# Performance work log

Measured on AMD Instinct MI355X. Metric: run time of the kernel, lower is better.

The kernel has to match this reference:

```python
import jax, jax.numpy as jnp
import numpy as np

B, S, DIM, H = 2, 2048, 1024, 16
DK = DIM // H  # 64
NEG = -10000000000.0


def setup_inputs() -> dict:
    key = jax.random.key(0)
    k1, k2, k3, k4, k5, k6 = jax.random.split(key, 6)
    dec_xs = jax.random.normal(k1, (B, S, DIM), dtype=jnp.float32)
    enc_xs = jax.random.normal(k2, (B, S, DIM), dtype=jnp.float32)
    mask = jax.random.randint(k3, (B, S, S), 0, 2, dtype=jnp.int32)
    # torch Linear weights: out = x @ W.T, bias=False
    sc = 1.0 / np.sqrt(DIM)
    Wq = jax.random.normal(k4, (DIM, DIM), dtype=jnp.float32) * sc
    Wkv = jax.random.normal(k5, (2 * DIM, DIM), dtype=jnp.float32) * sc
    Wo = jax.random.normal(k6, (DIM, DIM), dtype=jnp.float32) * sc
    return {"dec_xs": dec_xs, "enc_xs": enc_xs, "Wq": Wq, "Wkv": Wkv, "Wo": Wo, "mask": mask}


def reference(dec_xs, enc_xs, Wq, Wkv, Wo, mask):
    b, s, dim = enc_xs.shape
    qs = dec_xs @ Wq.T                      # [b,s,dim]  (dropout inactive in eval)
    kv = enc_xs @ Wkv.T                     # [b,s,2*dim]
    ks, vs = jnp.split(kv, 2, axis=-1)
    # head layout: view(b, s, dk, h) -- heads LAST, as in the original
    qs = qs.reshape(b, s, DK, H)
    ks = ks.reshape(b, s, DK, H)
    vs = vs.reshape(b, s, DK, H)
    scores = jnp.einsum('bqdh,bkdh->bqkh', qs, ks) / np.sqrt(DK)
    scores = jnp.where(mask[..., None] == 0, NEG, scores)
    weights = jax.nn.softmax(scores, axis=-2)  # softmax over key axis
    out = jnp.einsum('bqkh,bkdh->bqdh', weights, vs).reshape(b, s, dim)
    return out @ Wo.T
```

## Files before the change

kernel.cpp:

```cpp
#include <hip/hip_runtime.h>
#include <hip/hip_bf16.h>

#define BB 2
#define SS 2048
#define DIMM 1024
#define HH 16
#define DKK 64
#define QSCALE 0.18033688011112042592f

using bf16 = __hip_bfloat16;
typedef __attribute__((ext_vector_type(8))) short v8s;
typedef __attribute__((ext_vector_type(4))) short v4s;
typedef __attribute__((ext_vector_type(4))) float f32x4;

__device__ __forceinline__ void cvt4(const float* __restrict__ s,
                                     bf16* __restrict__ d, int idx) {
  const float4 f = ((const float4*)s)[idx];
  bf16 t[4] = {__float2bfloat16(f.x), __float2bfloat16(f.y),
               __float2bfloat16(f.z), __float2bfloat16(f.w)};
  *(v4s*)(d + (size_t)idx * 4) = *(const v4s*)t;
}

__global__ __launch_bounds__(256) void convert_pack_kernel(
    const float* __restrict__ dec, const float* __restrict__ enc,
    const float* __restrict__ Wq, const float* __restrict__ Wkv,
    const float* __restrict__ Wo, const int* __restrict__ mask,
    bf16* __restrict__ decb, bf16* __restrict__ encb, bf16* __restrict__ Wqb,
    bf16* __restrict__ Wkvb, bf16* __restrict__ Wob,
    unsigned long long* __restrict__ mp) {
  const int gid = blockIdx.x * 256 + threadIdx.x;
  const int NT = 256 * 1024;
#pragma unroll
  for (int i = 0; i < 4; ++i) cvt4(dec, decb, gid + i * NT);
#pragma unroll
  for (int i = 0; i < 4; ++i) cvt4(enc, encb, gid + i * NT);
  cvt4(Wq, Wqb, gid);
#pragma unroll
  for (int i = 0; i < 2; ++i) cvt4(Wkv, Wkvb, gid + i * NT);
  {
    const int n = gid >> 8;
    const int c4 = (gid & 255) * 4;
    const int h = c4 >> 6, d0 = c4 & 63;
    const float* src = Wo + (size_t)n * DIMM + h;
    bf16 t[4];
#pragma unroll
    for (int i2 = 0; i2 < 4; ++i2)
      t[i2] = __float2bfloat16(src[(d0 + i2) * 16]);
    *(v4s*)(Wob + (size_t)n * DIMM + c4) = *(const v4s*)t;
  }
  const int lane = threadIdx.x & 63;
  const int wave_id = gid >> 6;
  for (int i = 0; i < 32; ++i) {
    const size_t w = (size_t)wave_id * 32 + i;
    const unsigned long long bm = __ballot(mask[w * 64 + lane] != 0);
    if (lane == 0) mp[w] = bm;
  }
}

__global__ __launch_bounds__(256) void proj_gemm_kernel(
    const bf16* __restrict__ decb, const bf16* __restrict__ encb,
    const bf16* __restrict__ Wqb, const bf16* __restrict__ Wkvb,
    bf16* __restrict__ Qr, bf16* __restrict__ Kr, bf16* __restrict__ Vt) {
  __shared__ __align__(16) bf16 As[128][72];
  __shared__ __align__(16) bf16 Bs[128][72];
  const int t = threadIdx.x;
  const int wave = t >> 6, lane = t & 63;
  const int quad = lane >> 4, l15 = lane & 15;
  const int wm = (wave >> 1) * 64, wn = (wave & 1) * 64;
  const int bx = blockIdx.x;
  const int kind = bx >> 3;
  const int g = bx & 7;
  const int m0 = blockIdx.y * 128;

  const int sr = t >> 2;
  const int sc = (t & 3) * 16;
  const int voff = (kind == 2) ? DIMM : 0;
  const int wr0 = sr * 16 + g * 2 + voff;
  const int wr1 = sr * 16 + g * 2 + 1 + voff;

  const bf16* arow0;
  const bf16* arow1;
  const bf16* brow0;
  const bf16* brow1;
  if (kind == 0) {
    arow0 = decb + (size_t)(m0 + sr) * DIMM;
    arow1 = decb + (size_t)(m0 + sr + 64) * DIMM;
    brow0 = Wqb + (size_t)wr0 * DIMM;
    brow1 = Wqb + (size_t)wr1 * DIMM;
  } else if (kind == 1) {
    arow0 = encb + (size_t)(m0 + sr) * DIMM;
    arow1 = encb + (size_t)(m0 + sr + 64) * DIMM;
    brow0 = Wkvb + (size_t)wr0 * DIMM;
    brow1 = Wkvb + (size_t)wr1 * DIMM;
  } else {
    arow0 = Wkvb + (size_t)wr0 * DIMM;
    arow1 = Wkvb + (size_t)wr1 * DIMM;
    brow0 = encb + (size_t)(m0 + sr) * DIMM;
    brow1 = encb + (size_t)(m0 + sr + 64) * DIMM;
  }

  v8s apf[4], bpf[4];
  auto loadAB = [&](int kc) {
    apf[0] = ((const v8s*)(arow0 + kc + sc))[0];
    apf[1] = ((const v8s*)(arow0 + kc + sc))[1];
    apf[2] = ((const v8s*)(arow1 + kc + sc))[0];
    apf[3] = ((const v8s*)(arow1 + kc + sc))[1];
    bpf[0] = ((const v8s*)(brow0 + kc + sc))[0];
    bpf[1] = ((const v8s*)(brow0 + kc + sc))[1];
    bpf[2] = ((const v8s*)(brow1 + kc + sc))[0];
    bpf[3] = ((const v8s*)(brow1 + kc + sc))[1];
  };

  f32x4 acc[4][4] = {};
  loadAB(0);

  for (int kc = 0; kc < DIMM; kc += 64) {
    __syncthreads();
    *(v8s*)&As[sr][sc] = apf[0];
    *(v8s*)&As[sr][sc + 8] = apf[1];
    *(v8s*)&As[sr + 64][sc] = apf[2];
    *(v8s*)&As[sr + 64][sc + 8] = apf[3];
    *(v8s*)&Bs[sr][sc] = bpf[0];
    *(v8s*)&Bs[sr][sc + 8] = bpf[1];
    *(v8s*)&Bs[sr + 64][sc] = bpf[2];
    *(v8s*)&Bs[sr + 64][sc + 8] = bpf[3];
    if (kc + 64 < DIMM) loadAB(kc + 64);
    __syncthreads();
#pragma unroll
    for (int ks = 0; ks < 2; ++ks) {
      v8s af[4], bfr[4];
#pragma unroll
      for (int i = 0; i < 4; ++i)
        af[i] = *(const v8s*)&As[wm + i * 16 + l15][ks * 32 + quad * 8];
#pragma unroll
      for (int j = 0; j < 4; ++j)
        bfr[j] = *(const v8s*)&Bs[wn + j * 16 + l15][ks * 32 + quad * 8];
#pragma unroll
      for (int i = 0; i < 4; ++i)
#pragma unroll
        for (int j = 0; j < 4; ++j)
          acc[i][j] = __builtin_amdgcn_mfma_f32_16x16x32_bf16(
              af[i], bfr[j], acc[i][j], 0, 0, 0);
    }
  }

#pragma unroll
  for (int i = 0; i < 4; ++i) {
#pragma unroll
    for (int r = 0; r < 4; ++r) {
      const int mm = wm + i * 16 + quad * 4 + r;
#pragma unroll
      for (int j = 0; j < 4; ++j) {
        const int nn = wn + j * 16 + l15;
        const float v = acc[i][j][r];
        if (kind == 0) {
          Qr[(size_t)(m0 + mm) * DIMM + g * 128 + nn] =
              __float2bfloat16(v * QSCALE);
        } else if (kind == 1) {
          Kr[(size_t)(m0 + mm) * DIMM + g * 128 + nn] = __float2bfloat16(v);
        } else {
          const int h = g * 2 + (mm >> 6), d = mm & 63;
          const int sn = m0 + nn;
          const int b = sn >> 11, s = sn & (SS - 1);
          Vt[(((size_t)b * HH + h) * DKK + d) * SS + s] = __float2bfloat16(v);
        }
      }
    }
  }
}

__global__ __launch_bounds__(256) void out_gemm_kernel(
    const bf16* __restrict__ A, const bf16* __restrict__ W,
    float* __restrict__ out) {
  __shared__ __align__(16) bf16 As[128][72];
  __shared__ __align__(16) bf16 Bs[64][72];
  const int t = threadIdx.x;
  const int wave = t >> 6, lane = t & 63;
  const int quad = lane >> 4, l15 = lane & 15;
  const int wm = (wave >> 1) * 64, wn = (wave & 1) * 32;
  const int n0 = blockIdx.x * 64;
  const int m0 = blockIdx.y * 128;
  const int sr = t >> 2;
  const int sc = (t & 3) * 16;

  v8s ar[4], br[2];
  auto loadA = [&](int kc) {
#pragma unroll
    for (int rr = 0; rr < 2; ++rr) {
      const bf16* p = A + (size_t)(m0 + sr + rr * 64) * DIMM + kc + sc;
#pragma unroll
      for (int i = 0; i < 2; ++i) ar[rr * 2 + i] = ((const v8s*)p)[i];
    }
  };
  auto loadB = [&](int kc) {
    const bf16* p = W + (size_t)(n0 + sr) * DIMM + kc + sc;
#pragma unroll
    for (int i = 0; i < 2; ++i) br[i] = ((const v8s*)p)[i];
  };

  f32x4 acc[4][2] = {};
  loadA(0);
  loadB(0);
  for (int kc = 0; kc < DIMM; kc += 64) {
    __syncthreads();
#pragma unroll
    for (int rr = 0; rr < 2; ++rr) {
      *(v8s*)&As[sr + rr * 64][sc] = ar[rr * 2 + 0];
      *(v8s*)&As[sr + rr * 64][sc + 8] = ar[rr * 2 + 1];
    }
    *(v8s*)&Bs[sr][sc] = br[0];
    *(v8s*)&Bs[sr][sc + 8] = br[1];
    if (kc + 64 < DIMM) {
      loadA(kc + 64);
      loadB(kc + 64);
    }
    __syncthreads();
#pragma unroll
    for (int ks = 0; ks < 2; ++ks) {
      v8s af[4], bfr[2];
#pragma unroll
      for (int i = 0; i < 4; ++i)
        af[i] = *(const v8s*)&As[wm + i * 16 + l15][ks * 32 + quad * 8];
#pragma unroll
      for (int j = 0; j < 2; ++j)
        bfr[j] = *(const v8s*)&Bs[wn + j * 16 + l15][ks * 32 + quad * 8];
#pragma unroll
      for (int i = 0; i < 4; ++i)
#pragma unroll
        for (int j = 0; j < 2; ++j)
          acc[i][j] = __builtin_amdgcn_mfma_f32_16x16x32_bf16(
              af[i], bfr[j], acc[i][j], 0, 0, 0);
    }
  }

#pragma unroll
  for (int i = 0; i < 4; ++i) {
#pragma unroll
    for (int r = 0; r < 4; ++r) {
      const int m = m0 + wm + i * 16 + quad * 4 + r;
#pragma unroll
      for (int j = 0; j < 2; ++j) {
        const int n = n0 + wn + j * 16 + l15;
        out[(size_t)m * DIMM + n] = acc[i][j][r];
      }
    }
  }
}

__global__ __launch_bounds__(512) void attn_kernel(
    const bf16* __restrict__ Qr, const bf16* __restrict__ Kr,
    const bf16* __restrict__ Vt, const unsigned long long* __restrict__ mp,
    bf16* __restrict__ Ar) {
  __shared__ __align__(16) bf16 Ks[2][64][72];
  __shared__ __align__(16) bf16 Vs[2][64][72];
  __shared__ __align__(16) bf16 Ps[8][16][72];

  const int t = threadIdx.x;
  const int wave = t >> 6, lane = t & 63;
  const int quad = lane >> 4, l15 = lane & 15;

  const int bx = blockIdx.x;
  const int xcd = bx & 7, j = bx >> 3;
  const int g = (xcd << 2) | (j & 3);
  const int tile = j >> 2;
  const int h = g & 15, b = g >> 4;

  const int qw = tile * 128 + wave * 16;
  const size_t bhv = ((size_t)b * HH + h) * DKK;

  const bf16* qrow = Qr + ((size_t)(b * SS + qw + l15)) * DIMM + h * 64;
  const v8s aq0 = *(const v8s*)(qrow + quad * 8);
  const v8s aq1 = *(const v8s*)(qrow + 32 + quad * 8);

  f32x4 o[4] = {};
  float lsum[4] = {0.f, 0.f, 0.f, 0.f};

  const int id0 = t * 8;
  const int r0 = id0 >> 6, c0 = id0 & 63;

  auto loadK = [&](int kt) {
    return *(const v8s*)(Kr + ((size_t)(b * SS + kt * 64 + r0)) * DIMM +
                         h * 64 + c0);
  };
  auto loadV = [&](int kt) {
    return *(const v8s*)(Vt + (bhv + r0) * SS + kt * 64 + c0);
  };

  v8s kreg = loadK(0), vreg = loadV(0);
  *(v8s*)&Ks[0][r0][c0] = kreg;
  *(v8s*)&Vs[0][r0][c0] = vreg;
  kreg = loadK(1);
  vreg = loadV(1);

  int p = 0;
  for (int kt = 0; kt < 32; ++kt) {
    __syncthreads();
    if (kt < 31) {
      *(v8s*)&Ks[p ^ 1][r0][c0] = kreg;
      *(v8s*)&Vs[p ^ 1][r0][c0] = vreg;
      if (kt < 30) {
        kreg = loadK(kt + 2);
        vreg = loadV(kt + 2);
      }
    }

    unsigned long long mw[4];
#pragma unroll
    for (int r = 0; r < 4; ++r)
      mw[r] = mp[((size_t)b * SS + qw + quad * 4 + r) * 32 + kt] >> l15;

    f32x4 sc[4];
#pragma unroll
    for (int n = 0; n < 4; ++n) {
      const v8s bk0 = *(const v8s*)&Ks[p][n * 16 + l15][quad * 8];
      const v8s bk1 = *(const v8s*)&Ks[p][n * 16 + l15][32 + quad * 8];
      f32x4 z = {0.f, 0.f, 0.f, 0.f};
      z = __builtin_amdgcn_mfma_f32_16x16x32_bf16(aq0, bk0, z, 0, 0, 0);
      sc[n] = __builtin_amdgcn_mfma_f32_16x16x32_bf16(aq1, bk1, z, 0, 0, 0);
    }

#pragma unroll
    for (int n = 0; n < 4; ++n)
#pragma unroll
      for (int r = 0; r < 4; ++r) {
        const bool keep = (mw[r] >> (n * 16)) & 1ULL;
        const float pw = keep ? __builtin_amdgcn_exp2f(sc[n][r]) : 0.f;
        sc[n][r] = pw;
        lsum[r] += pw;
      }

#pragma unroll
    for (int n = 0; n < 4; ++n)
#pragma unroll
      for (int r = 0; r < 4; ++r)
        Ps[wave][quad * 4 + r][n * 16 + l15] = __float2bfloat16(sc[n][r]);
    const v8s ap0 = *(const v8s*)&Ps[wave][l15][quad * 8];
    const v8s ap1 = *(const v8s*)&Ps[wave][l15][32 + quad * 8];

#pragma unroll
    for (int n = 0; n < 4; ++n) {
      const v8s bv0 = *(const v8s*)&Vs[p][n * 16 + l15][quad * 8];
      const v8s bv1 = *(const v8s*)&Vs[p][n * 16 + l15][32 + quad * 8];
      o[n] = __builtin_amdgcn_mfma_f32_16x16x32_bf16(ap0, bv0, o[n], 0, 0, 0);
      o[n] = __builtin_amdgcn_mfma_f32_16x16x32_bf16(ap1, bv1, o[n], 0, 0, 0);
    }
    p ^= 1;
  }

#pragma unroll
  for (int r = 0; r < 4; ++r) {
    float l = lsum[r];
    l += __shfl_xor(l, 1);
    l += __shfl_xor(l, 2);
    l += __shfl_xor(l, 4);
    l += __shfl_xor(l, 8);
    const float inv = 1.f / l;
    const size_t row = (size_t)b * SS + qw + quad * 4 + r;
#pragma unroll
    for (int n = 0; n < 4; ++n) {
      Ar[row * DIMM + h * 64 + n * 16 + l15] = __float2bfloat16(o[n][r] * inv);
    }
  }
}

extern "C" void kernel_launch(void* const* d_in, const int* in_sizes, int n_in,
                              void* d_out, int out_size, void* d_ws,
                              size_t ws_size, hipStream_t stream) {
  const float* dec = (const float*)d_in[0];
  const float* enc = (const float*)d_in[1];
  const float* Wq = (const float*)d_in[2];
  const float* Wkv = (const float*)d_in[3];
  const float* Wo = (const float*)d_in[4];
  const int* mask = (const int*)d_in[5];
  float* out = (float*)d_out;

  bf16* decb = (bf16*)d_out;
  bf16* Wqb = (bf16*)((char*)d_out + ((size_t)2 * SS * DIMM * 2));

  char* ws = (char*)d_ws;
  size_t off = 0;
  bf16* encb = (bf16*)(ws + off);
  bf16* Ar = (bf16*)(ws + off);   off += (size_t)2 * SS * DIMM * 2;
  bf16* Wkvb = (bf16*)(ws + off); off += (size_t)2 * DIMM * DIMM * 2;
  bf16* Wob = (bf16*)(ws + off);  off += (size_t)DIMM * DIMM * 2;
  bf16* Qr = (bf16*)(ws + off);   off += (size_t)2 * SS * DIMM * 2;
  bf16* Kr = (bf16*)(ws + off);   off += (size_t)2 * SS * DIMM * 2;
  bf16* Vt = (bf16*)(ws + off);   off += (size_t)2 * SS * DIMM * 2;
  unsigned long long* mp = (unsigned long long*)(ws + off);

  dim3 blk(256);
  convert_pack_kernel<<<dim3(1024), blk, 0, stream>>>(
      dec, enc, Wq, Wkv, Wo, mask, decb, encb, Wqb, Wkvb, Wob, mp);
  proj_gemm_kernel<<<dim3(24, 32), blk, 0, stream>>>(decb, encb, Wqb, Wkvb, Qr,
                                                     Kr, Vt);
  attn_kernel<<<dim3(512), dim3(512), 0, stream>>>(Qr, Kr, Vt, mp, Ar);
  out_gemm_kernel<<<dim3(16, 32), blk, 0, stream>>>(Ar, Wob, out);
}
```

Before: 255.5 us.

## Load K/V fragments straight from global memory and halve attention block size

The attention kernel no longer stages K and V tiles through double-buffered shared memory with block-wide barriers. Each wave now loads its MFMA operand fragments directly from global memory (relying on L2/L1 reuse), and the block is shrunk to 4 waves with twice as many blocks. This removes the __syncthreads and LDS traffic and improves occupancy, but each wave now issues redundant global loads for the same K/V tile and has no software prefetch, so latency may be exposed.

```diff
diff --git a/kernel.cpp b/kernel.cpp
--- a/kernel.cpp
+++ b/kernel.cpp
@@ -247,13 +247,11 @@
   }
 }
 
-__global__ __launch_bounds__(512) void attn_kernel(
+__global__ __launch_bounds__(256) void attn_kernel(
     const bf16* __restrict__ Qr, const bf16* __restrict__ Kr,
     const bf16* __restrict__ Vt, const unsigned long long* __restrict__ mp,
     bf16* __restrict__ Ar) {
-  __shared__ __align__(16) bf16 Ks[2][64][72];
-  __shared__ __align__(16) bf16 Vs[2][64][72];
-  __shared__ __align__(16) bf16 Ps[8][16][72];
+  __shared__ __align__(16) bf16 Ps[4][16][72];
 
   const int t = threadIdx.x;
   const int wave = t >> 6, lane = t & 63;
@@ -265,45 +263,32 @@
   const int tile = j >> 2;
   const int h = g & 15, b = g >> 4;
 
-  const int qw = tile * 128 + wave * 16;
+  const int qw = tile * 64 + wave * 16;
   const size_t bhv = ((size_t)b * HH + h) * DKK;
 
   const bf16* qrow = Qr + ((size_t)(b * SS + qw + l15)) * DIMM + h * 64;
   const v8s aq0 = *(const v8s*)(qrow + quad * 8);
   const v8s aq1 = *(const v8s*)(qrow + 32 + quad * 8);
 
+  const bf16* kbase = Kr + ((size_t)b * SS) * DIMM + h * 64 + quad * 8;
+  const bf16* vbase = Vt + bhv * SS;
+
   f32x4 o[4] = {};
   float lsum[4] = {0.f, 0.f, 0.f, 0.f};
 
-  const int id0 = t * 8;
-  const int r0 = id0 >> 6, c0 = id0 & 63;
-
-  auto loadK = [&](int kt) {
-    return *(const v8s*)(Kr + ((size_t)(b * SS + kt * 64 + r0)) * DIMM +
-                         h * 64 + c0);
-  };
-  auto loadV = [&](int kt) {
-    return *(const v8s*)(Vt + (bhv + r0) * SS + kt * 64 + c0);
-  };
-
-  v8s kreg = loadK(0), vreg = loadV(0);
-  *(v8s*)&Ks[0][r0][c0] = kreg;
-  *(v8s*)&Vs[0][r0][c0] = vreg;
-  kreg = loadK(1);
-  vreg = loadV(1);
-
-  int p = 0;
   for (int kt = 0; kt < 32; ++kt) {
-    __syncthreads();
-    if (kt < 31) {
-      *(v8s*)&Ks[p ^ 1][r0][c0] = kreg;
-      *(v8s*)&Vs[p ^ 1][r0][c0] = vreg;
-      if (kt < 30) {
-        kreg = loadK(kt + 2);
-        vreg = loadV(kt + 2);
-      }
-    }
-
+    const int k0 = kt * 64;
+
+    v8s bk[4][2], bv[4][2];
+#pragma unroll
+    for (int n = 0; n < 4; ++n) {
+      const bf16* kr = kbase + (size_t)(k0 + n * 16 + l15) * DIMM;
+      bk[n][0] = *(const v8s*)kr;
+      bk[n][1] = *(const v8s*)(kr + 32);
+      const bf16* vr = vbase + (size_t)(n * 16 + l15) * SS + k0 + quad * 8;
+      bv[n][0] = *(const v8s*)vr;
+      bv[n][1] = *(const v8s*)(vr + 32);
+    }
     unsigned long long mw[4];
 #pragma unroll
     for (int r = 0; r < 4; ++r)
@@ -312,11 +297,10 @@
     f32x4 sc[4];
 #pragma unroll
     for (int n = 0; n < 4; ++n) {
-      const v8s bk0 = *(const v8s*)&Ks[p][n * 16 + l15][quad * 8];
-      const v8s bk1 = *(const v8s*)&Ks[p][n * 16 + l15][32 + quad * 8];
       f32x4 z = {0.f, 0.f, 0.f, 0.f};
-      z = __builtin_amdgcn_mfma_f32_16x16x32_bf16(aq0, bk0, z, 0, 0, 0);
-      sc[n] = __builtin_amdgcn_mfma_f32_16x16x32_bf16(aq1, bk1, z, 0, 0, 0);
+      z = __builtin_amdgcn_mfma_f32_16x16x32_bf16(aq0, bk[n][0], z, 0, 0, 0);
+      sc[n] =
+          __builtin_amdgcn_mfma_f32_16x16x32_bf16(aq1, bk[n][1], z, 0, 0, 0);
     }
 
 #pragma unroll
@@ -339,12 +323,11 @@
 
 #pragma unroll
     for (int n = 0; n < 4; ++n) {
-      const v8s bv0 = *(const v8s*)&Vs[p][n * 16 + l15][quad * 8];
-      const v8s bv1 = *(const v8s*)&Vs[p][n * 16 + l15][32 + quad * 8];
-      o[n] = __builtin_amdgcn_mfma_f32_16x16x32_bf16(ap0, bv0, o[n], 0, 0, 0);
-      o[n] = __builtin_amdgcn_mfma_f32_16x16x32_bf16(ap1, bv1, o[n], 0, 0, 0);
-    }
-    p ^= 1;
+      o[n] =
+          __builtin_amdgcn_mfma_f32_16x16x32_bf16(ap0, bv[n][0], o[n], 0, 0, 0);
+      o[n] =
+          __builtin_amdgcn_mfma_f32_16x16x32_bf16(ap1, bv[n][1], o[n], 0, 0, 0);
+    }
   }
 
 #pragma unroll
@@ -393,6 +376,6 @@
       dec, enc, Wq, Wkv, Wo, mask, decb, encb, Wqb, Wkvb, Wob, mp);
   proj_gemm_kernel<<<dim3(24, 32), blk, 0, stream>>>(decb, encb, Wqb, Wkvb, Qr,
                                                      Kr, Vt);
-  attn_kernel<<<dim3(512), dim3(512), 0, stream>>>(Qr, Kr, Vt, mp, Ar);
+  attn_kernel<<<dim3(1024), blk, 0, stream>>>(Qr, Kr, Vt, mp, Ar);
   out_gemm_kernel<<<dim3(16, 32), blk, 0, stream>>>(Ar, Wob, out);
 }
```

New measurement: 427.3 us. +67.3%, slower.
